# Performance work log

Hardware: AMD Instinct MI355X
Metric: run time of the kernel (lower is better)

The kernel has to match this reference:

```python
import jax, jax.numpy as jnp
import numpy as np

B, T, C = 2, 2048, 1024
NH = 16
HD = C // NH

def setup_inputs() -> dict:
    key = jax.random.key(0)
    ks = jax.random.split(key, 4)
    x = jax.random.normal(ks[0], (B, T, C), dtype=jnp.float32)
    w_attn = jax.random.normal(ks[1], (C, 3 * C), dtype=jnp.float32) * (1.0 / np.sqrt(C))
    b_attn = jnp.zeros((3 * C,), dtype=jnp.float32)
    w_proj = jax.random.normal(ks[2], (C, C), dtype=jnp.float32) * (1.0 / np.sqrt(C))
    b_proj = jnp.zeros((C,), dtype=jnp.float32)
    return {"x": x, "w_attn": w_attn, "b_attn": b_attn, "w_proj": w_proj, "b_proj": b_proj}

def reference(x, w_attn, b_attn, w_proj, b_proj):
    Bq, Tq, Cq = x.shape
    qkv = x @ w_attn + b_attn                      # [B,T,3C]
    q, k, v = jnp.split(qkv, 3, axis=2)
    # [B,T,C] -> [B,NH,T,HD]
    def heads(t):
        return t.reshape(Bq, Tq, NH, HD).transpose(0, 2, 1, 3)
    q, k, v = heads(q), heads(k), heads(v)
    att = jnp.einsum('bhqd,bhkd->bhqk', q, k) * (1.0 / np.sqrt(HD))
    causal = jnp.tril(jnp.ones((Tq, Tq), dtype=bool))
    att = jnp.where(causal[None, None], att, -jnp.inf)
    att = jax.nn.softmax(att, axis=-1)
    y = jnp.einsum('bhqk,bhkd->bhqd', att, v)      # [B,NH,T,HD]
    y = y.transpose(0, 2, 1, 3).reshape(Bq, Tq, Cq)
    return y @ w_proj + b_proj
```

## Files before the change

### kernel.cpp

```cpp
#include <hip/hip_runtime.h>

typedef unsigned short u16;
typedef short bf16x8 __attribute__((ext_vector_type(8)));
typedef float f32x4 __attribute__((ext_vector_type(4)));

#define BATCH 2
#define SEQ   2048
#define CH    1024
#define NHEAD 16
#define HDIM  64
#define ROWS  (BATCH*SEQ)

#define WAITV(N) asm volatile("s_waitcnt vmcnt(" #N ")" ::: "memory")

__device__ __forceinline__ u16 f2b(float f) {
  unsigned u = __builtin_bit_cast(unsigned, f);
  u += 0x7FFFu + ((u >> 16) & 1u);
  return (u16)(u >> 16);
}
__device__ __forceinline__ float b2f(u16 h) {
  unsigned u = ((unsigned)h) << 16;
  return __builtin_bit_cast(float, u);
}
__device__ __forceinline__ float exp2_fast(float x) {
  float r; asm("v_exp_f32 %0, %1" : "=v"(r) : "v"(x)); return r;
}
__device__ __forceinline__ unsigned cvt_pk_bf16(float a, float b) {
  unsigned r; asm("v_cvt_pk_bf16_f32 %0, %1, %2" : "=v"(r) : "v"(a), "v"(b)); return r;
}

__device__ __forceinline__ void gload_lds16(const void* g, void* l) {
  __builtin_amdgcn_global_load_lds(
      (const __attribute__((address_space(1))) unsigned int*)g,
      (__attribute__((address_space(3))) unsigned int*)l, 16, 0, 0);
}

__global__ void csa_prep(const float* __restrict__ x,
                         const float* __restrict__ wa, const float* __restrict__ wp,
                         u16* __restrict__ xb, u16* __restrict__ wat,
                         u16* __restrict__ wpt) {
  __shared__ float tile[32][33];
  const int b = blockIdx.x, t = threadIdx.x;
  if (b < 2048) {
    int i = b * 256 + t;
    const float4* f4 = (const float4*)x;
    float4 v0 = f4[2*i], v1 = f4[2*i+1];
    ushort4 o0, o1;
    o0.x = f2b(v0.x); o0.y = f2b(v0.y); o0.z = f2b(v0.z); o0.w = f2b(v0.w);
    o1.x = f2b(v1.x); o1.y = f2b(v1.y); o1.z = f2b(v1.z); o1.w = f2b(v1.w);
    ((ushort4*)xb)[2*i]   = o0;
    ((ushort4*)xb)[2*i+1] = o1;
    return;
  }
  int bb = b - 2048;
  int bx = bb & 127, by = bb >> 7;
  const float* in; u16* out; int C;
  if (bx < 96) { in = wa; out = wat; C = 3*CH; }
  else         { in = wp; out = wpt; C = CH; bx -= 96; }
  const int R = CH;
  const int bxc = bx * 32, byc = by * 32;
  const int tx = t & 31, ty = t >> 5;
  #pragma unroll
  for (int j = 0; j < 4; ++j) {
    int r = byc + ty + j*8, c = bxc + tx;
    tile[ty + j*8][tx] = in[(size_t)r*C + c];
  }
  __syncthreads();
  #pragma unroll
  for (int j = 0; j < 4; ++j) {
    int oc = bxc + ty + j*8;
    int orr = byc + tx;
    out[(size_t)oc*R + orr] = f2b(tile[tx][ty + j*8]);
  }
}

__global__ __launch_bounds__(512) void csa_gemm_qkv(
    const u16* __restrict__ A, const u16* __restrict__ Bt,
    const float* __restrict__ bias,
    u16* __restrict__ qbo, u16* __restrict__ kb, u16* __restrict__ vtb)
{
  __shared__ __align__(16) u16 As[3][256*64];
  __shared__ __align__(16) u16 Bs[2][192*64];
  const int t = threadIdx.x, lane = t & 63, w = t >> 6;
  const int wm = w >> 2, wn = w & 3, g = lane >> 4, qi = lane & 15;
  const int xq = (qi & 7) * 8;

  const int wgid = blockIdx.y * 16 + blockIdx.x;
  const int c8 = wgid & 7, inner = wgid >> 3;
  const int bm = (c8 >> 1) * 4 + (inner >> 3);
  const int bn = (c8 & 1) * 8 + (inner & 7);

  f32x4 acc[8][3] = {};

  const u16* Ab = A  + (size_t)(bm*256)*CH;
  const u16* Bb = Bt + (size_t)(bn*192)*CH;
  const int srow = t >> 3;
  const int scolsw = ((t & 7) * 8) ^ ((srow & 7) * 8);

#define QKV_STAGE_A(kt_, buf_) do { const size_t k_ = (size_t)(kt_)*64;            \
    gload_lds16(Ab + (size_t)(  0 + srow)*CH + k_ + scolsw, &As[buf_][      w*512]); \
    gload_lds16(Ab + (size_t)( 64 + srow)*CH + k_ + scolsw, &As[buf_][ 4096+w*512]); \
    gload_lds16(Ab + (size_t)(128 + srow)*CH + k_ + scolsw, &As[buf_][ 8192+w*512]); \
    gload_lds16(Ab + (size_t)(192 + srow)*CH + k_ + scolsw, &As[buf_][12288+w*512]); \
  } while (0)
#define QKV_STAGE_B(kt_, buf_) do { const size_t k_ = (size_t)(kt_)*64;            \
    gload_lds16(Bb + (size_t)(  0 + srow)*CH + k_ + scolsw, &Bs[buf_][      w*512]); \
    gload_lds16(Bb + (size_t)( 64 + srow)*CH + k_ + scolsw, &Bs[buf_][ 4096+w*512]); \
    gload_lds16(Bb + (size_t)(128 + srow)*CH + k_ + scolsw, &Bs[buf_][ 8192+w*512]); \
  } while (0)

  QKV_STAGE_A(0, 0); QKV_STAGE_B(0, 0); QKV_STAGE_A(1, 1);

  int a3 = 0;
  for (int kt = 0; kt < 16; ++kt) {
    if (kt < 15) QKV_STAGE_B(kt + 1, (kt + 1) & 1);
    if (kt < 14) { int ab = a3 + 2; if (ab >= 3) ab -= 3; QKV_STAGE_A(kt + 2, ab); }
    if (kt < 14)       WAITV(11);
    else if (kt == 14) WAITV(7);
    else               WAITV(0);
    __builtin_amdgcn_s_barrier();
    __builtin_amdgcn_sched_barrier(0);
    const u16* Ac = &As[a3][0];
    const u16* Bc = &Bs[kt & 1][0];
    #pragma unroll
    for (int kk = 0; kk < 2; ++kk) {
      bf16x8 af[8], bfr[3];
      #pragma unroll
      for (int m = 0; m < 8; ++m)
        af[m] = *(const bf16x8*)&Ac[(wm*128 + m*16 + qi)*64 + ((kk*32 + g*8) ^ xq)];
      #pragma unroll
      for (int n = 0; n < 3; ++n)
        bfr[n] = *(const bf16x8*)&Bc[(wn*48 + n*16 + qi)*64 + ((kk*32 + g*8) ^ xq)];
      #pragma unroll
      for (int m = 0; m < 8; ++m)
        #pragma unroll
        for (int n = 0; n < 3; ++n)
          acc[m][n] = __builtin_amdgcn_mfma_f32_16x16x32_bf16(af[m], bfr[n], acc[m][n], 0, 0, 0);
    }
    __builtin_amdgcn_s_barrier();
    a3 = (a3 == 2) ? 0 : a3 + 1;
  }
#undef QKV_STAGE_A
#undef QKV_STAGE_B

  #pragma unroll
  for (int m = 0; m < 8; ++m) {
    const int row0 = bm*256 + wm*128 + m*16 + g*4;
    const int bb = row0 >> 11;
    const int t0 = row0 & 2047;
    #pragma unroll
    for (int n = 0; n < 3; ++n) {
      const int col = bn*192 + wn*48 + n*16 + qi;
      const float bv = bias[col];
      const int which = col >> 10;
      const int cc = col & 1023;
      const int h = cc >> 6, d = cc & 63;
      const int bh = bb*16 + h;
      if (which == 2) {
        ushort4 pw;
        pw.x = f2b(acc[m][n][0] + bv);
        pw.y = f2b(acc[m][n][1] + bv);
        pw.z = f2b(acc[m][n][2] + bv);
        pw.w = f2b(acc[m][n][3] + bv);
        *(ushort4*)&vtb[((size_t)bh*HDIM + d)*SEQ + t0] = pw;
      } else {
        u16* dst = (which == 0) ? qbo : kb;
        #pragma unroll
        for (int r = 0; r < 4; ++r)
          dst[((size_t)bh*SEQ + t0 + r)*HDIM + d] = f2b(acc[m][n][r] + bv);
      }
    }
  }
}

__global__ __launch_bounds__(256) void csa_gemm_proj(
    const u16* __restrict__ A, const u16* __restrict__ Bt,
    const float* __restrict__ bias, float* __restrict__ out)
{
  __shared__ __align__(16) u16 As[3][128*64];
  __shared__ __align__(16) u16 Bs[2][128*64];
  const int t = threadIdx.x, lane = t & 63, w = t >> 6;
  const int wm = w >> 1, wn = w & 1, g = lane >> 4, qi = lane & 15;
  const int xq = (qi & 7) * 8;
  const int bm = blockIdx.y, bn = blockIdx.x;

  f32x4 acc[4][4] = {};

  const u16* Ab = A  + (size_t)(bm*128)*CH;
  const u16* Bb = Bt + (size_t)(bn*128)*CH;
  const int srow = t >> 3;
  const int scolsw = ((t & 7) * 8) ^ ((srow & 7) * 8);

#define PRJ_STAGE(P_, base_, kt_, buf_) do { const size_t k_ = (size_t)(kt_)*64;      \
    gload_lds16(P_ + (size_t)( 0 + srow)*CH + k_ + scolsw, &base_[buf_][     w*512]); \
    gload_lds16(P_ + (size_t)(32 + srow)*CH + k_ + scolsw, &base_[buf_][2048+w*512]); \
    gload_lds16(P_ + (size_t)(64 + srow)*CH + k_ + scolsw, &base_[buf_][4096+w*512]); \
    gload_lds16(P_ + (size_t)(96 + srow)*CH + k_ + scolsw, &base_[buf_][6144+w*512]); \
  } while (0)

  PRJ_STAGE(Ab, As, 0, 0); PRJ_STAGE(Bb, Bs, 0, 0); PRJ_STAGE(Ab, As, 1, 1);

  int a3 = 0;
  for (int kt = 0; kt < 16; ++kt) {
    if (kt < 15) PRJ_STAGE(Bb, Bs, kt + 1, (kt + 1) & 1);
    if (kt < 14) { int ab = a3 + 2; if (ab >= 3) ab -= 3; PRJ_STAGE(Ab, As, kt + 2, ab); }
    if (kt < 14)       WAITV(12);
    else if (kt == 14) WAITV(8);
    else               WAITV(0);
    __builtin_amdgcn_s_barrier();
    __builtin_amdgcn_sched_barrier(0);
    const u16* Ac = &As[a3][0];
    const u16* Bc = &Bs[kt & 1][0];
    #pragma unroll
    for (int kk = 0; kk < 2; ++kk) {
      bf16x8 af[4], bfr[4];
      #pragma unroll
      for (int m = 0; m < 4; ++m)
        af[m] = *(const bf16x8*)&Ac[(wm*64 + m*16 + qi)*64 + ((kk*32 + g*8) ^ xq)];
      #pragma unroll
      for (int n = 0; n < 4; ++n)
        bfr[n] = *(const bf16x8*)&Bc[(wn*64 + n*16 + qi)*64 + ((kk*32 + g*8) ^ xq)];
      #pragma unroll
      for (int m = 0; m < 4; ++m)
        #pragma unroll
        for (int n = 0; n < 4; ++n)
          acc[m][n] = __builtin_amdgcn_mfma_f32_16x16x32_bf16(af[m], bfr[n], acc[m][n], 0, 0, 0);
    }
    __builtin_amdgcn_s_barrier();
    a3 = (a3 == 2) ? 0 : a3 + 1;
  }
#undef PRJ_STAGE

  #pragma unroll
  for (int m = 0; m < 4; ++m) {
    const int row0 = bm*128 + wm*64 + m*16 + g*4;
    #pragma unroll
    for (int n = 0; n < 4; ++n) {
      const int col = bn*128 + wn*64 + n*16 + qi;
      const float bv = bias[col];
      #pragma unroll
      for (int r = 0; r < 4; ++r)
        out[(size_t)(row0 + r)*CH + col] = acc[m][n][r] + bv;
    }
  }
}

__global__ __launch_bounds__(512) void csa_attn(
    const u16* __restrict__ qb, const u16* __restrict__ kb,
    const u16* __restrict__ vtb, u16* __restrict__ yout)
{
  const int bh = blockIdx.x, pair = blockIdx.y;
  const int bidx = bh >> 4, h = bh & 15;
  const int t = threadIdx.x, lane = t & 63, w = t >> 6;
  const int g = lane >> 4, qi = lane & 15;
  __shared__ __align__(16) u16 Ks[2][128*64];
  __shared__ __align__(16) u16 Vs[2][64*128];
  __shared__ __align__(16) u16 Ps[8][2][16*64];

  const size_t kvbase = (size_t)bh * SEQ * HDIM;
  const u16* kb_bh  = kb  + kvbase;
  const u16* vtb_bh = vtb + kvbase;

  const int krow_  = t >> 3;
  const int kcolsw = ((t & 7) * 8) ^ ((krow_ & 7) * 8);
  const int vd_    = t >> 4;
  const int vcolsw = ((t & 15) * 8) ^ ((vd_ & 15) * 8);

  int offKb[2][4], offVb[2][4], offPw[4], offPr[2];
  #pragma unroll
  for (int c = 0; c < 2; ++c) {
    offPr[c] = qi*64 + ((c*32 + g*8) ^ ((qi & 7) * 8));
    #pragma unroll
    for (int s4 = 0; s4 < 4; ++s4)
      offKb[c][s4] = (s4*16 + qi)*64 + ((c*32 + g*8) ^ ((qi & 7) * 8));
    #pragma unroll
    for (int nf = 0; nf < 4; ++nf)
      offVb[c][nf] = (nf*16 + qi)*128 + ((c*32 + g*8) ^ (qi * 8));
  }
  #pragma unroll
  for (int s4 = 0; s4 < 4; ++s4)
    offPw[s4] = qi*64 + ((s4*16 + g*4) ^ ((qi & 7) * 8));

  const float QSCALE = 0.18033688011112042f;
  const int lqa = w*16 + qi;

  for (int half = 0; half < 2; ++half) {
    const int qt = half ? (15 - pair) : pair;
    const int qrow = qt*128 + w*16;
    const int ntile = qt + 1;

    bf16x8 qf[2];
    #pragma unroll
    for (int c = 0; c < 2; ++c) {
      qf[c] = *(const bf16x8*)&qb[(kvbase + (size_t)(qrow + qi)*HDIM) + c*32 + g*8];
      #pragma unroll
      for (int e = 0; e < 8; ++e)
        qf[c][e] = (short)f2b(b2f((u16)qf[c][e]) * QSCALE);
    }

    f32x4 yacc[4] = {};
    float mrun = -1e30f, srun = 0.f;

    __syncthreads();
    {
      const u16* kp = kb_bh;
      gload_lds16(kp + (size_t)krow_*64 + kcolsw,        &Ks[0][       w*512]);
      gload_lds16(kp + (size_t)(64 + krow_)*64 + kcolsw, &Ks[0][4096 + w*512]);
      const u16* vp = vtb_bh;
      gload_lds16(vp + (size_t)vd_*SEQ + vcolsw,         &Vs[0][       w*512]);
      gload_lds16(vp + (size_t)(32 + vd_)*SEQ + vcolsw,  &Vs[0][4096 + w*512]);
    }
    __syncthreads();

    int buf = 0;
    for (int kt = 0; kt < ntile; ++kt) {
      if (kt + 1 < ntile) {
        const u16* kp = kb_bh + (size_t)((kt + 1) * 128) * 64;
        gload_lds16(kp + (size_t)krow_*64 + kcolsw,        &Ks[buf^1][       w*512]);
        gload_lds16(kp + (size_t)(64 + krow_)*64 + kcolsw, &Ks[buf^1][4096 + w*512]);
        const u16* vp = vtb_bh + (kt + 1) * 128;
        gload_lds16(vp + (size_t)vd_*SEQ + vcolsw,         &Vs[buf^1][       w*512]);
        gload_lds16(vp + (size_t)(32 + vd_)*SEQ + vcolsw,  &Vs[buf^1][4096 + w*512]);
      }

      f32x4 sa[4] = {}, sb[4] = {};
      #pragma unroll
      for (int c = 0; c < 2; ++c)
        #pragma unroll
        for (int s4 = 0; s4 < 4; ++s4) {
          bf16x8 ka = *(const bf16x8*)&Ks[buf][offKb[c][s4]];
          sa[s4] = __builtin_amdgcn_mfma_f32_16x16x32_bf16(ka, qf[c], sa[s4], 0, 0, 0);
        }
      #pragma unroll
      for (int c = 0; c < 2; ++c)
        #pragma unroll
        for (int s4 = 0; s4 < 4; ++s4) {
          bf16x8 kbv = *(const bf16x8*)&Ks[buf][4096 + offKb[c][s4]];
          sb[s4] = __builtin_amdgcn_mfma_f32_16x16x32_bf16(kbv, qf[c], sb[s4], 0, 0, 0);
        }

      if (kt == ntile - 1) {
        #pragma unroll
        for (int s4 = 0; s4 < 4; ++s4)
          #pragma unroll
          for (int r = 0; r < 4; ++r) {
            const int lk = s4*16 + g*4 + r;
            if (lk > lqa)      sa[s4][r] = -3.0e38f;
            if (lk > lqa - 64) sb[s4][r] = -3.0e38f;
          }
      }

      float tmax = sa[0][0];
      #pragma unroll
      for (int s4 = 0; s4 < 4; ++s4)
        #pragma unroll
        for (int r = 0; r < 4; ++r) {
          tmax = fmaxf(tmax, sa[s4][r]);
          tmax = fmaxf(tmax, sb[s4][r]);
        }
      if (!__all(tmax - mrun <= 11.5f)) {
        float tmf = fmaxf(tmax, __shfl_xor(tmax, 16));
        tmf = fmaxf(tmf, __shfl_xor(tmf, 32));
        float mnew = fmaxf(mrun, tmf);
        float fac = exp2_fast(mrun - mnew);
        #pragma unroll
        for (int r = 0; r < 4; ++r) {
          float fr = __shfl(fac, g*4 + r);
          #pragma unroll
          for (int nf = 0; nf < 4; ++nf) yacc[nf][r] *= fr;
        }
        srun *= fac;
        mrun = mnew;
      }
      float tsum = 0.f;
      #pragma unroll
      for (int s4 = 0; s4 < 4; ++s4)
        #pragma unroll
        for (int r = 0; r < 4; ++r) {
          float pa = exp2_fast(sa[s4][r] - mrun);
          float pb = exp2_fast(sb[s4][r] - mrun);
          sa[s4][r] = pa; sb[s4][r] = pb;
          tsum += pa + pb;
        }
      srun += tsum;

      #pragma unroll
      for (int s4 = 0; s4 < 4; ++s4) {
        uint2 pwa, pwb;
        pwa.x = cvt_pk_bf16(sa[s4][0], sa[s4][1]);
        pwa.y = cvt_pk_bf16(sa[s4][2], sa[s4][3]);
        pwb.x = cvt_pk_bf16(sb[s4][0], sb[s4][1]);
        pwb.y = cvt_pk_bf16(sb[s4][2], sb[s4][3]);
        *(uint2*)&Ps[w][0][offPw[s4]] = pwa;
        *(uint2*)&Ps[w][1][offPw[s4]] = pwb;
      }

      #pragma unroll
      for (int c = 0; c < 2; ++c) {
        bf16x8 pa0 = *(const bf16x8*)&Ps[w][0][offPr[c]];
        bf16x8 pb0 = *(const bf16x8*)&Ps[w][1][offPr[c]];
        #pragma unroll
        for (int nf = 0; nf < 4; ++nf) {
          bf16x8 va = *(const bf16x8*)&Vs[buf][offVb[c][nf]];
          yacc[nf] = __builtin_amdgcn_mfma_f32_16x16x32_bf16(pa0, va, yacc[nf], 0, 0, 0);
          bf16x8 vb = *(const bf16x8*)&Vs[buf][offVb[c][nf] ^ 64];
          yacc[nf] = __builtin_amdgcn_mfma_f32_16x16x32_bf16(pb0, vb, yacc[nf], 0, 0, 0);
        }
      }

      __syncthreads();
      buf ^= 1;
    }

    float srf = srun + __shfl_xor(srun, 16);
    srf += __shfl_xor(srf, 32);
    #pragma unroll
    for (int r = 0; r < 4; ++r) {
      float sv = __shfl(srf, g*4 + r);
      float inv = 1.f / sv;
      int qg = qrow + g*4 + r;
      #pragma unroll
      for (int nf = 0; nf < 4; ++nf) {
        int d = nf*16 + qi;
        yout[((size_t)bidx*SEQ + qg)*CH + h*HDIM + d] = f2b(yacc[nf][r] * inv);
      }
    }
  }
}

extern "C" void kernel_launch(void* const* d_in, const int* in_sizes, int n_in,
                              void* d_out, int out_size, void* d_ws, size_t ws_size,
                              hipStream_t stream) {
  (void)in_sizes; (void)n_in; (void)out_size; (void)ws_size;
  const float* x      = (const float*)d_in[0];
  const float* w_attn = (const float*)d_in[1];
  const float* b_attn = (const float*)d_in[2];
  const float* w_proj = (const float*)d_in[3];
  const float* b_proj = (const float*)d_in[4];

  char* ws = (char*)d_ws;
  const size_t MB = 1024*1024;
  u16* xb  = (u16*)(ws);
  u16* wat = (u16*)(ws +  8*MB);
  u16* wpt = (u16*)(ws + 14*MB);
  u16* qb  = (u16*)(ws + 16*MB);
  u16* kb  = (u16*)(ws + 24*MB);
  u16* vtb = (u16*)(ws + 32*MB);

  csa_prep<<<6144, 256, 0, stream>>>(x, w_attn, w_proj, xb, wat, wpt);
  csa_gemm_qkv<<<dim3(16, 16), 512, 0, stream>>>(xb, wat, b_attn, qb, kb, vtb);
  csa_attn<<<dim3(32, 8), 512, 0, stream>>>(qb, kb, vtb, xb);
  csa_gemm_proj<<<dim3(8, 32), 256, 0, stream>>>(xb, wpt, b_proj, (float*)d_out);
}
```

Baseline: 99.24 us.

## Triple-buffer attention K/V tiles with vmcnt waits and MFMA priority boosts

Result: no change. 100.5 us (+1.2%).

```diff
diff --git a/kernel.cpp b/kernel.cpp
--- a/kernel.cpp
+++ b/kernel.cpp
@@ -253,8 +253,8 @@
   const int bidx = bh >> 4, h = bh & 15;
   const int t = threadIdx.x, lane = t & 63, w = t >> 6;
   const int g = lane >> 4, qi = lane & 15;
-  __shared__ __align__(16) u16 Ks[2][128*64];
-  __shared__ __align__(16) u16 Vs[2][64*128];
+  __shared__ __align__(16) u16 Ks[3][128*64];
+  __shared__ __align__(16) u16 Vs[3][64*128];
   __shared__ __align__(16) u16 Ps[8][2][16*64];
 
   const size_t kvbase = (size_t)bh * SEQ * HDIM;
@@ -266,6 +266,15 @@
   const int vd_    = t >> 4;
   const int vcolsw = ((t & 15) * 8) ^ ((vd_ & 15) * 8);
 
+#define ATTN_STAGE(kt_, buf_) do {                                                  \
+    const u16* kp_ = kb_bh + (size_t)((kt_) * 128) * 64;                            \
+    gload_lds16(kp_ + (size_t)krow_*64 + kcolsw,        &Ks[buf_][       w*512]);   \
+    gload_lds16(kp_ + (size_t)(64 + krow_)*64 + kcolsw, &Ks[buf_][4096 + w*512]);   \
+    const u16* vp_ = vtb_bh + (kt_) * 128;                                          \
+    gload_lds16(vp_ + (size_t)vd_*SEQ + vcolsw,         &Vs[buf_][       w*512]);   \
+    gload_lds16(vp_ + (size_t)(32 + vd_)*SEQ + vcolsw,  &Vs[buf_][4096 + w*512]);   \
+  } while (0)
+
   int offKb[2][4], offVb[2][4], offPw[4], offPr[2];
   #pragma unroll
   for (int c = 0; c < 2; ++c) {
@@ -301,43 +310,38 @@
     f32x4 yacc[4] = {};
     float mrun = -1e30f, srun = 0.f;
 
-    __syncthreads();
-    {
-      const u16* kp = kb_bh;
-      gload_lds16(kp + (size_t)krow_*64 + kcolsw,        &Ks[0][       w*512]);
-      gload_lds16(kp + (size_t)(64 + krow_)*64 + kcolsw, &Ks[0][4096 + w*512]);
-      const u16* vp = vtb_bh;
-      gload_lds16(vp + (size_t)vd_*SEQ + vcolsw,         &Vs[0][       w*512]);
-      gload_lds16(vp + (size_t)(32 + vd_)*SEQ + vcolsw,  &Vs[0][4096 + w*512]);
-    }
-    __syncthreads();
-
-    int buf = 0;
+    ATTN_STAGE(0, 0);
+    if (ntile > 1) ATTN_STAGE(1, 1);
+
+    int cur = 0;
     for (int kt = 0; kt < ntile; ++kt) {
-      if (kt + 1 < ntile) {
-        const u16* kp = kb_bh + (size_t)((kt + 1) * 128) * 64;
-        gload_lds16(kp + (size_t)krow_*64 + kcolsw,        &Ks[buf^1][       w*512]);
-        gload_lds16(kp + (size_t)(64 + krow_)*64 + kcolsw, &Ks[buf^1][4096 + w*512]);
-        const u16* vp = vtb_bh + (kt + 1) * 128;
-        gload_lds16(vp + (size_t)vd_*SEQ + vcolsw,         &Vs[buf^1][       w*512]);
-        gload_lds16(vp + (size_t)(32 + vd_)*SEQ + vcolsw,  &Vs[buf^1][4096 + w*512]);
-      }
+      {
+        int b2 = cur + 2; if (b2 >= 3) b2 -= 3;
+        if (kt + 2 < ntile) ATTN_STAGE(kt + 2, b2);
+      }
+      if (kt + 2 < ntile)      WAITV(8);
+      else if (kt + 1 < ntile) WAITV(4);
+      else                     WAITV(0);
+      __builtin_amdgcn_s_barrier();
+      __builtin_amdgcn_sched_barrier(0);
 
       f32x4 sa[4] = {}, sb[4] = {};
+      __builtin_amdgcn_s_setprio(1);
       #pragma unroll
       for (int c = 0; c < 2; ++c)
         #pragma unroll
         for (int s4 = 0; s4 < 4; ++s4) {
-          bf16x8 ka = *(const bf16x8*)&Ks[buf][offKb[c][s4]];
+          bf16x8 ka = *(const bf16x8*)&Ks[cur][offKb[c][s4]];
           sa[s4] = __builtin_amdgcn_mfma_f32_16x16x32_bf16(ka, qf[c], sa[s4], 0, 0, 0);
         }
       #pragma unroll
       for (int c = 0; c < 2; ++c)
         #pragma unroll
         for (int s4 = 0; s4 < 4; ++s4) {
-          bf16x8 kbv = *(const bf16x8*)&Ks[buf][4096 + offKb[c][s4]];
+          bf16x8 kbv = *(const bf16x8*)&Ks[cur][4096 + offKb[c][s4]];
           sb[s4] = __builtin_amdgcn_mfma_f32_16x16x32_bf16(kbv, qf[c], sb[s4], 0, 0, 0);
         }
+      __builtin_amdgcn_s_setprio(0);
 
       if (kt == ntile - 1) {
         #pragma unroll
@@ -395,22 +399,25 @@
         *(uint2*)&Ps[w][1][offPw[s4]] = pwb;
       }
 
+      __builtin_amdgcn_s_setprio(1);
       #pragma unroll
       for (int c = 0; c < 2; ++c) {
         bf16x8 pa0 = *(const bf16x8*)&Ps[w][0][offPr[c]];
         bf16x8 pb0 = *(const bf16x8*)&Ps[w][1][offPr[c]];
         #pragma unroll
         for (int nf = 0; nf < 4; ++nf) {
-          bf16x8 va = *(const bf16x8*)&Vs[buf][offVb[c][nf]];
+          bf16x8 va = *(const bf16x8*)&Vs[cur][offVb[c][nf]];
           yacc[nf] = __builtin_amdgcn_mfma_f32_16x16x32_bf16(pa0, va, yacc[nf], 0, 0, 0);
-          bf16x8 vb = *(const bf16x8*)&Vs[buf][offVb[c][nf] ^ 64];
+          bf16x8 vb = *(const bf16x8*)&Vs[cur][offVb[c][nf] ^ 64];
           yacc[nf] = __builtin_amdgcn_mfma_f32_16x16x32_bf16(pb0, vb, yacc[nf], 0, 0, 0);
         }
       }
-
-      __syncthreads();
-      buf ^= 1;
-    }
+      __builtin_amdgcn_s_setprio(0);
+
+      __builtin_amdgcn_s_barrier();
+      cur = (cur == 2) ? 0 : cur + 1;
+    }
+#undef ATTN_STAGE
 
     float srf = srun + __shfl_xor(srun, 16);
     srf += __shfl_xor(srf, 32);
```

## Rework attention kernel with 32x32 MFMA, register P, and split-KV wave pairs

Applied to the files above, without the earlier changes.

New measurement: 104.9 us. +5.7%, slower.

```diff
diff --git a/kernel.cpp b/kernel.cpp
--- a/kernel.cpp
+++ b/kernel.cpp
@@ -3,6 +3,7 @@
 typedef unsigned short u16;
 typedef short bf16x8 __attribute__((ext_vector_type(8)));
 typedef float f32x4 __attribute__((ext_vector_type(4)));
+typedef float f32x16 __attribute__((ext_vector_type(16)));
 
 #define BATCH 2
 #define SEQ   2048
@@ -252,180 +253,180 @@
   const int bh = blockIdx.x, pair = blockIdx.y;
   const int bidx = bh >> 4, h = bh & 15;
   const int t = threadIdx.x, lane = t & 63, w = t >> 6;
-  const int g = lane >> 4, qi = lane & 15;
+  const int j = w >> 1, sub = w & 1;
+  const int l31 = lane & 31, hi = lane >> 5;
+
   __shared__ __align__(16) u16 Ks[2][128*64];
   __shared__ __align__(16) u16 Vs[2][64*128];
-  __shared__ __align__(16) u16 Ps[8][2][16*64];
+  __shared__ float mtab[8][32], stab[8][32], ftab[8][32];
 
   const size_t kvbase = (size_t)bh * SEQ * HDIM;
   const u16* kb_bh  = kb  + kvbase;
   const u16* vtb_bh = vtb + kvbase;
 
-  const int krow_  = t >> 3;
-  const int kcolsw = ((t & 7) * 8) ^ ((krow_ & 7) * 8);
-  const int vd_    = t >> 4;
-  const int vcolsw = ((t & 15) * 8) ^ ((vd_ & 15) * 8);
-
-  int offKb[2][4], offVb[2][4], offPw[4], offPr[2];
-  #pragma unroll
-  for (int c = 0; c < 2; ++c) {
-    offPr[c] = qi*64 + ((c*32 + g*8) ^ ((qi & 7) * 8));
-    #pragma unroll
-    for (int s4 = 0; s4 < 4; ++s4)
-      offKb[c][s4] = (s4*16 + qi)*64 + ((c*32 + g*8) ^ ((qi & 7) * 8));
-    #pragma unroll
-    for (int nf = 0; nf < 4; ++nf)
-      offVb[c][nf] = (nf*16 + qi)*128 + ((c*32 + g*8) ^ (qi * 8));
-  }
-  #pragma unroll
-  for (int s4 = 0; s4 < 4; ++s4)
-    offPw[s4] = qi*64 + ((s4*16 + g*4) ^ ((qi & 7) * 8));
+  const int krow = t >> 3;
+  const int kcol = 8 * ((t & 7) ^ (krow & 7));
+  const int vrow = t >> 4;
+  const int vcol = 8 * ((t & 15) ^ (vrow & 15));
+
+#define ATTN_STAGE(kt_, b_) do {                                             \
+    const u16* kp_ = kb_bh + (size_t)((kt_)*128 + krow)*64 + kcol;           \
+    gload_lds16(kp_,           &Ks[b_][       w*512]);                       \
+    gload_lds16(kp_ + 64*64,   &Ks[b_][4096 + w*512]);                       \
+    const u16* vp_ = vtb_bh + (size_t)vrow*SEQ + (kt_)*128 + vcol;           \
+    gload_lds16(vp_,           &Vs[b_][       w*512]);                       \
+    gload_lds16(vp_ + 32*SEQ,  &Vs[b_][4096 + w*512]);                       \
+  } while (0)
+
+  int offK[2][4];
+  #pragma unroll
+  for (int kb2 = 0; kb2 < 2; ++kb2)
+    #pragma unroll
+    for (int ds = 0; ds < 4; ++ds)
+      offK[kb2][ds] = (sub*64 + kb2*32 + l31)*64 + ((ds*16 + hi*8) ^ ((l31 & 7)*8));
+  int offV[2][4];
+  #pragma unroll
+  for (int db = 0; db < 2; ++db)
+    #pragma unroll
+    for (int ks = 0; ks < 4; ++ks)
+      offV[db][ks] = (db*32 + l31)*128 + (((sub*8 + 2*ks + hi) ^ (l31 & 15))*8);
+
+#define PACK(ps_, b_, out_) do {                                             \
+    unsigned A0_ = cvt_pk_bf16(ps_[(b_)+0], ps_[(b_)+1]);                    \
+    unsigned A1_ = cvt_pk_bf16(ps_[(b_)+2], ps_[(b_)+3]);                    \
+    unsigned B0_ = cvt_pk_bf16(ps_[(b_)+4], ps_[(b_)+5]);                    \
+    unsigned B1_ = cvt_pk_bf16(ps_[(b_)+6], ps_[(b_)+7]);                    \
+    asm volatile("v_permlane32_swap_b32 %0, %1" : "+v"(A0_), "+v"(B0_));     \
+    asm volatile("v_permlane32_swap_b32 %0, %1" : "+v"(A1_), "+v"(B1_));     \
+    union { unsigned u[4]; bf16x8 v; } pu_;                                  \
+    pu_.u[0] = A0_; pu_.u[1] = A1_; pu_.u[2] = B0_; pu_.u[3] = B1_;          \
+    out_ = pu_.v;                                                            \
+  } while (0)
 
   const float QSCALE = 0.18033688011112042f;
-  const int lqa = w*16 + qi;
+  const int qloc = j*32 + l31;
 
   for (int half = 0; half < 2; ++half) {
     const int qt = half ? (15 - pair) : pair;
-    const int qrow = qt*128 + w*16;
     const int ntile = qt + 1;
-
-    bf16x8 qf[2];
-    #pragma unroll
-    for (int c = 0; c < 2; ++c) {
-      qf[c] = *(const bf16x8*)&qb[(kvbase + (size_t)(qrow + qi)*HDIM) + c*32 + g*8];
+    const int qrow = qt*128 + j*32;
+
+    bf16x8 qf[4];
+    #pragma unroll
+    for (int ds = 0; ds < 4; ++ds) {
+      qf[ds] = *(const bf16x8*)&qb[kvbase + (size_t)(qrow + l31)*HDIM + ds*16 + hi*8];
       #pragma unroll
       for (int e = 0; e < 8; ++e)
-        qf[c][e] = (short)f2b(b2f((u16)qf[c][e]) * QSCALE);
-    }
-
-    f32x4 yacc[4] = {};
+        qf[ds][e] = (short)f2b(b2f((u16)qf[ds][e]) * QSCALE);
+    }
+
+    f32x16 yacc0 = {}, yacc1 = {};
     float mrun = -1e30f, srun = 0.f;
 
-    __syncthreads();
-    {
-      const u16* kp = kb_bh;
-      gload_lds16(kp + (size_t)krow_*64 + kcolsw,        &Ks[0][       w*512]);
-      gload_lds16(kp + (size_t)(64 + krow_)*64 + kcolsw, &Ks[0][4096 + w*512]);
-      const u16* vp = vtb_bh;
-      gload_lds16(vp + (size_t)vd_*SEQ + vcolsw,         &Vs[0][       w*512]);
-      gload_lds16(vp + (size_t)(32 + vd_)*SEQ + vcolsw,  &Vs[0][4096 + w*512]);
-    }
+    ATTN_STAGE(0, 0);
     __syncthreads();
 
     int buf = 0;
     for (int kt = 0; kt < ntile; ++kt) {
-      if (kt + 1 < ntile) {
-        const u16* kp = kb_bh + (size_t)((kt + 1) * 128) * 64;
-        gload_lds16(kp + (size_t)krow_*64 + kcolsw,        &Ks[buf^1][       w*512]);
-        gload_lds16(kp + (size_t)(64 + krow_)*64 + kcolsw, &Ks[buf^1][4096 + w*512]);
-        const u16* vp = vtb_bh + (kt + 1) * 128;
-        gload_lds16(vp + (size_t)vd_*SEQ + vcolsw,         &Vs[buf^1][       w*512]);
-        gload_lds16(vp + (size_t)(32 + vd_)*SEQ + vcolsw,  &Vs[buf^1][4096 + w*512]);
-      }
-
-      f32x4 sa[4] = {}, sb[4] = {};
-      #pragma unroll
-      for (int c = 0; c < 2; ++c)
-        #pragma unroll
-        for (int s4 = 0; s4 < 4; ++s4) {
-          bf16x8 ka = *(const bf16x8*)&Ks[buf][offKb[c][s4]];
-          sa[s4] = __builtin_amdgcn_mfma_f32_16x16x32_bf16(ka, qf[c], sa[s4], 0, 0, 0);
-        }
-      #pragma unroll
-      for (int c = 0; c < 2; ++c)
-        #pragma unroll
-        for (int s4 = 0; s4 < 4; ++s4) {
-          bf16x8 kbv = *(const bf16x8*)&Ks[buf][4096 + offKb[c][s4]];
-          sb[s4] = __builtin_amdgcn_mfma_f32_16x16x32_bf16(kbv, qf[c], sb[s4], 0, 0, 0);
-        }
+      if (kt + 1 < ntile) ATTN_STAGE(kt + 1, buf ^ 1);
+
+      f32x16 s0 = {}, s1 = {};
+      #pragma unroll
+      for (int ds = 0; ds < 4; ++ds) {
+        bf16x8 k0 = *(const bf16x8*)&Ks[buf][offK[0][ds]];
+        s0 = __builtin_amdgcn_mfma_f32_32x32x16_bf16(k0, qf[ds], s0, 0, 0, 0);
+        bf16x8 k1 = *(const bf16x8*)&Ks[buf][offK[1][ds]];
+        s1 = __builtin_amdgcn_mfma_f32_32x32x16_bf16(k1, qf[ds], s1, 0, 0, 0);
+      }
 
       if (kt == ntile - 1) {
         #pragma unroll
-        for (int s4 = 0; s4 < 4; ++s4)
-          #pragma unroll
-          for (int r = 0; r < 4; ++r) {
-            const int lk = s4*16 + g*4 + r;
-            if (lk > lqa)      sa[s4][r] = -3.0e38f;
-            if (lk > lqa - 64) sb[s4][r] = -3.0e38f;
-          }
-      }
-
-      float tmax = sa[0][0];
-      #pragma unroll
-      for (int s4 = 0; s4 < 4; ++s4)
-        #pragma unroll
-        for (int r = 0; r < 4; ++r) {
-          tmax = fmaxf(tmax, sa[s4][r]);
-          tmax = fmaxf(tmax, sb[s4][r]);
+        for (int reg = 0; reg < 16; ++reg) {
+          const int cr = (reg & 3) + 8*(reg >> 2) + 4*hi;
+          if (sub*64 + cr > qloc)      s0[reg] = -3.0e38f;
+          if (sub*64 + 32 + cr > qloc) s1[reg] = -3.0e38f;
         }
+      }
+
+      float tmax = fmaxf(s0[0], s1[0]);
+      #pragma unroll
+      for (int reg = 1; reg < 16; ++reg)
+        tmax = fmaxf(tmax, fmaxf(s0[reg], s1[reg]));
       if (!__all(tmax - mrun <= 11.5f)) {
-        float tmf = fmaxf(tmax, __shfl_xor(tmax, 16));
-        tmf = fmaxf(tmf, __shfl_xor(tmf, 32));
+        float tmf = fmaxf(tmax, __shfl_xor(tmax, 32));
         float mnew = fmaxf(mrun, tmf);
         float fac = exp2_fast(mrun - mnew);
+        if (lane < 32) ftab[w][l31] = fac;
         #pragma unroll
-        for (int r = 0; r < 4; ++r) {
-          float fr = __shfl(fac, g*4 + r);
-          #pragma unroll
-          for (int nf = 0; nf < 4; ++nf) yacc[nf][r] *= fr;
+        for (int reg = 0; reg < 16; ++reg) {
+          float fr = ftab[w][(reg & 3) + 8*(reg >> 2) + 4*hi];
+          yacc0[reg] *= fr; yacc1[reg] *= fr;
         }
-        srun *= fac;
-        mrun = mnew;
+        srun *= fac; mrun = mnew;
       }
       float tsum = 0.f;
       #pragma unroll
-      for (int s4 = 0; s4 < 4; ++s4)
-        #pragma unroll
-        for (int r = 0; r < 4; ++r) {
-          float pa = exp2_fast(sa[s4][r] - mrun);
-          float pb = exp2_fast(sb[s4][r] - mrun);
-          sa[s4][r] = pa; sb[s4][r] = pb;
-          tsum += pa + pb;
-        }
+      for (int reg = 0; reg < 16; ++reg) {
+        float p0 = exp2_fast(s0[reg] - mrun);
+        float p1 = exp2_fast(s1[reg] - mrun);
+        s0[reg] = p0; s1[reg] = p1;
+        tsum += p0 + p1;
+      }
       srun += tsum;
 
-      #pragma unroll
-      for (int s4 = 0; s4 < 4; ++s4) {
-        uint2 pwa, pwb;
-        pwa.x = cvt_pk_bf16(sa[s4][0], sa[s4][1]);
-        pwa.y = cvt_pk_bf16(sa[s4][2], sa[s4][3]);
-        pwb.x = cvt_pk_bf16(sb[s4][0], sb[s4][1]);
-        pwb.y = cvt_pk_bf16(sb[s4][2], sb[s4][3]);
-        *(uint2*)&Ps[w][0][offPw[s4]] = pwa;
-        *(uint2*)&Ps[w][1][offPw[s4]] = pwb;
-      }
-
-      #pragma unroll
-      for (int c = 0; c < 2; ++c) {
-        bf16x8 pa0 = *(const bf16x8*)&Ps[w][0][offPr[c]];
-        bf16x8 pb0 = *(const bf16x8*)&Ps[w][1][offPr[c]];
-        #pragma unroll
-        for (int nf = 0; nf < 4; ++nf) {
-          bf16x8 va = *(const bf16x8*)&Vs[buf][offVb[c][nf]];
-          yacc[nf] = __builtin_amdgcn_mfma_f32_16x16x32_bf16(pa0, va, yacc[nf], 0, 0, 0);
-          bf16x8 vb = *(const bf16x8*)&Vs[buf][offVb[c][nf] ^ 64];
-          yacc[nf] = __builtin_amdgcn_mfma_f32_16x16x32_bf16(pb0, vb, yacc[nf], 0, 0, 0);
-        }
-      }
+      bf16x8 pa0, pa1, pa2, pa3;
+      PACK(s0, 0, pa0); PACK(s0, 8, pa1); PACK(s1, 0, pa2); PACK(s1, 8, pa3);
+
+      yacc0 = __builtin_amdgcn_mfma_f32_32x32x16_bf16(pa0, *(const bf16x8*)&Vs[buf][offV[0][0]], yacc0, 0, 0, 0);
+      yacc0 = __builtin_amdgcn_mfma_f32_32x32x16_bf16(pa1, *(const bf16x8*)&Vs[buf][offV[0][1]], yacc0, 0, 0, 0);
+      yacc0 = __builtin_amdgcn_mfma_f32_32x32x16_bf16(pa2, *(const bf16x8*)&Vs[buf][offV[0][2]], yacc0, 0, 0, 0);
+      yacc0 = __builtin_amdgcn_mfma_f32_32x32x16_bf16(pa3, *(const bf16x8*)&Vs[buf][offV[0][3]], yacc0, 0, 0, 0);
+      yacc1 = __builtin_amdgcn_mfma_f32_32x32x16_bf16(pa0, *(const bf16x8*)&Vs[buf][offV[1][0]], yacc1, 0, 0, 0);
+      yacc1 = __builtin_amdgcn_mfma_f32_32x32x16_bf16(pa1, *(const bf16x8*)&Vs[buf][offV[1][1]], yacc1, 0, 0, 0);
+      yacc1 = __builtin_amdgcn_mfma_f32_32x32x16_bf16(pa2, *(const bf16x8*)&Vs[buf][offV[1][2]], yacc1, 0, 0, 0);
+      yacc1 = __builtin_amdgcn_mfma_f32_32x32x16_bf16(pa3, *(const bf16x8*)&Vs[buf][offV[1][3]], yacc1, 0, 0, 0);
 
       __syncthreads();
       buf ^= 1;
     }
 
-    float srf = srun + __shfl_xor(srun, 16);
-    srf += __shfl_xor(srf, 32);
-    #pragma unroll
-    for (int r = 0; r < 4; ++r) {
-      float sv = __shfl(srf, g*4 + r);
-      float inv = 1.f / sv;
-      int qg = qrow + g*4 + r;
-      #pragma unroll
-      for (int nf = 0; nf < 4; ++nf) {
-        int d = nf*16 + qi;
-        yout[((size_t)bidx*SEQ + qg)*CH + h*HDIM + d] = f2b(yacc[nf][r] * inv);
-      }
-    }
-  }
+    float sfull = srun + __shfl_xor(srun, 32);
+    if (lane < 32) { mtab[w][l31] = mrun; stab[w][l31] = sfull; }
+    __syncthreads();
+
+    float* Ocomb = (float*)&Ks[0][0];
+    const int wA = w & ~1, wB = w | 1;
+    if (sub == 1) {
+      #pragma unroll
+      for (int reg = 0; reg < 16; ++reg) {
+        const int cr = (reg & 3) + 8*(reg >> 2) + 4*hi;
+        float mA = mtab[wA][cr], mB = mtab[wB][cr];
+        float fB = exp2_fast(mB - fmaxf(mA, mB));
+        Ocomb[(j*32 + cr)*64 +      l31] = yacc0[reg] * fB;
+        Ocomb[(j*32 + cr)*64 + 32 + l31] = yacc1[reg] * fB;
+      }
+    }
+    __syncthreads();
+    if (sub == 0) {
+      #pragma unroll
+      for (int reg = 0; reg < 16; ++reg) {
+        const int cr = (reg & 3) + 8*(reg >> 2) + 4*hi;
+        float mA = mtab[wA][cr], mB = mtab[wB][cr];
+        float sA = stab[wA][cr], sB = stab[wB][cr];
+        float ms = fmaxf(mA, mB);
+        float fA = exp2_fast(mA - ms), fB = exp2_fast(mB - ms);
+        float inv = 1.f / (sA * fA + sB * fB);
+        const size_t orow = ((size_t)bidx*SEQ + qt*128 + j*32 + cr)*CH + h*HDIM;
+        float v0 = (yacc0[reg] * fA + Ocomb[(j*32 + cr)*64 +      l31]) * inv;
+        float v1 = (yacc1[reg] * fA + Ocomb[(j*32 + cr)*64 + 32 + l31]) * inv;
+        yout[orow +      l31] = f2b(v0);
+        yout[orow + 32 + l31] = f2b(v1);
+      }
+    }
+    __syncthreads();
+  }
+#undef ATTN_STAGE
+#undef PACK
 }
 
 extern "C" void kernel_launch(void* const* d_in, const int* in_sizes, int n_in,
```

## Widen attention KV tile to 256 keys with single reusable P buffer

Applied to the files above, without the earlier changes.

Result: slower. 104.3 us (+5.1%).

```diff
diff --git a/kernel.cpp b/kernel.cpp
--- a/kernel.cpp
+++ b/kernel.cpp
@@ -253,33 +253,53 @@
   const int bidx = bh >> 4, h = bh & 15;
   const int t = threadIdx.x, lane = t & 63, w = t >> 6;
   const int g = lane >> 4, qi = lane & 15;
-  __shared__ __align__(16) u16 Ks[2][128*64];
-  __shared__ __align__(16) u16 Vs[2][64*128];
-  __shared__ __align__(16) u16 Ps[8][2][16*64];
+  __shared__ __align__(16) u16 Ks[2][256*64];
+  __shared__ __align__(16) u16 Vs[2][64*256];
+  __shared__ __align__(16) u16 Ps[8][16*64];
 
   const size_t kvbase = (size_t)bh * SEQ * HDIM;
   const u16* kb_bh  = kb  + kvbase;
   const u16* vtb_bh = vtb + kvbase;
 
-  const int krow_  = t >> 3;
-  const int kcolsw = ((t & 7) * 8) ^ ((krow_ & 7) * 8);
-  const int vd_    = t >> 4;
-  const int vcolsw = ((t & 15) * 8) ^ ((vd_ & 15) * 8);
-
-  int offKb[2][4], offVb[2][4], offPw[4], offPr[2];
+  const int krow4  = t >> 3;
+  const int kcolsw = ((t & 7) * 8) ^ ((krow4 & 7) * 8);
+  const int vrow16 = t >> 5;
+  const int vcolsw0 = 8 * ((t & 31) ^ vrow16);
+  const int vcolsw1 = 8 * ((t & 31) ^ (16 + vrow16));
+
+#define ATTN_STAGE(kbase_, b_) do {                                               \
+    const u16* kp_ = kb_bh + (size_t)((kbase_) + krow4)*64;                       \
+    gload_lds16(kp_ +            kcolsw, &Ks[b_][       w*512]);                  \
+    gload_lds16(kp_ +  64*64  + kcolsw, &Ks[b_][ 4096 + w*512]);                  \
+    gload_lds16(kp_ + 128*64  + kcolsw, &Ks[b_][ 8192 + w*512]);                  \
+    gload_lds16(kp_ + 192*64  + kcolsw, &Ks[b_][12288 + w*512]);                  \
+    const u16* vp_ = vtb_bh + (size_t)vrow16*SEQ + (kbase_);                      \
+    gload_lds16(vp_ +           vcolsw0, &Vs[b_][       w*512]);                  \
+    gload_lds16(vp_ + 16*SEQ + vcolsw1, &Vs[b_][ 4096 + w*512]);                  \
+    gload_lds16(vp_ + 32*SEQ + vcolsw0, &Vs[b_][ 8192 + w*512]);                  \
+    gload_lds16(vp_ + 48*SEQ + vcolsw1, &Vs[b_][12288 + w*512]);                  \
+  } while (0)
+
+  int offKb[2][4], offPw[4], offPr[2];
   #pragma unroll
   for (int c = 0; c < 2; ++c) {
     offPr[c] = qi*64 + ((c*32 + g*8) ^ ((qi & 7) * 8));
     #pragma unroll
     for (int s4 = 0; s4 < 4; ++s4)
       offKb[c][s4] = (s4*16 + qi)*64 + ((c*32 + g*8) ^ ((qi & 7) * 8));
-    #pragma unroll
-    for (int nf = 0; nf < 4; ++nf)
-      offVb[c][nf] = (nf*16 + qi)*128 + ((c*32 + g*8) ^ (qi * 8));
   }
   #pragma unroll
   for (int s4 = 0; s4 < 4; ++s4)
     offPw[s4] = qi*64 + ((s4*16 + g*4) ^ ((qi & 7) * 8));
+  int offVb[4][2][4];
+  #pragma unroll
+  for (int s = 0; s < 4; ++s)
+    #pragma unroll
+    for (int c = 0; c < 2; ++c)
+      #pragma unroll
+      for (int nf = 0; nf < 4; ++nf)
+        offVb[s][c][nf] = (nf*16 + qi)*256 +
+                          (((s*8 + c*4 + g) ^ (((nf & 1)*16) + qi)) * 8);
 
   const float QSCALE = 0.18033688011112042f;
   const int lqa = w*16 + qi;
@@ -287,7 +307,7 @@
   for (int half = 0; half < 2; ++half) {
     const int qt = half ? (15 - pair) : pair;
     const int qrow = qt*128 + w*16;
-    const int ntile = qt + 1;
+    const int ntile = (qt + 2) >> 1;
 
     bf16x8 qf[2];
     #pragma unroll
@@ -300,64 +320,56 @@
 
     f32x4 yacc[4] = {};
     float mrun = -1e30f, srun = 0.f;
+    const int dq = 128*qt - 256*(ntile - 1) + lqa;
 
     __syncthreads();
-    {
-      const u16* kp = kb_bh;
-      gload_lds16(kp + (size_t)krow_*64 + kcolsw,        &Ks[0][       w*512]);
-      gload_lds16(kp + (size_t)(64 + krow_)*64 + kcolsw, &Ks[0][4096 + w*512]);
-      const u16* vp = vtb_bh;
-      gload_lds16(vp + (size_t)vd_*SEQ + vcolsw,         &Vs[0][       w*512]);
-      gload_lds16(vp + (size_t)(32 + vd_)*SEQ + vcolsw,  &Vs[0][4096 + w*512]);
-    }
+    ATTN_STAGE(0, 0);
     __syncthreads();
 
     int buf = 0;
     for (int kt = 0; kt < ntile; ++kt) {
-      if (kt + 1 < ntile) {
-        const u16* kp = kb_bh + (size_t)((kt + 1) * 128) * 64;
-        gload_lds16(kp + (size_t)krow_*64 + kcolsw,        &Ks[buf^1][       w*512]);
-        gload_lds16(kp + (size_t)(64 + krow_)*64 + kcolsw, &Ks[buf^1][4096 + w*512]);
-        const u16* vp = vtb_bh + (kt + 1) * 128;
-        gload_lds16(vp + (size_t)vd_*SEQ + vcolsw,         &Vs[buf^1][       w*512]);
-        gload_lds16(vp + (size_t)(32 + vd_)*SEQ + vcolsw,  &Vs[buf^1][4096 + w*512]);
+      if (kt + 1 < ntile) ATTN_STAGE((kt + 1) * 256, buf ^ 1);
+
+      f32x4 S[4][4];
+      #pragma unroll
+      for (int s = 0; s < 4; ++s)
+        #pragma unroll
+        for (int s4 = 0; s4 < 4; ++s4)
+          S[s][s4] = (f32x4){0.f, 0.f, 0.f, 0.f};
+      #pragma unroll
+      for (int s = 0; s < 4; ++s)
+        #pragma unroll
+        for (int c = 0; c < 2; ++c)
+          #pragma unroll
+          for (int s4 = 0; s4 < 4; ++s4) {
+            bf16x8 kf = *(const bf16x8*)&Ks[buf][s*4096 + offKb[c][s4]];
+            S[s][s4] = __builtin_amdgcn_mfma_f32_16x16x32_bf16(kf, qf[c], S[s][s4], 0, 0, 0);
+          }
+
+      if (kt == ntile - 1) {
+        #pragma unroll
+        for (int s = 0; s < 4; ++s)
+          #pragma unroll
+          for (int s4 = 0; s4 < 4; ++s4)
+            #pragma unroll
+            for (int r = 0; r < 4; ++r) {
+              const int lkrel = s*64 + s4*16 + g*4 + r;
+              if (lkrel > dq) S[s][s4][r] = -3.0e38f;
+            }
       }
 
-      f32x4 sa[4] = {}, sb[4] = {};
-      #pragma unroll
-      for (int c = 0; c < 2; ++c)
+      float a0 = S[0][0][0], a1 = S[0][0][1], a2 = S[0][0][2], a3 = S[0][0][3];
+      #pragma unroll
+      for (int s = 0; s < 4; ++s)
         #pragma unroll
         for (int s4 = 0; s4 < 4; ++s4) {
-          bf16x8 ka = *(const bf16x8*)&Ks[buf][offKb[c][s4]];
-          sa[s4] = __builtin_amdgcn_mfma_f32_16x16x32_bf16(ka, qf[c], sa[s4], 0, 0, 0);
+          if (s == 0 && s4 == 0) continue;
+          a0 = fmaxf(a0, S[s][s4][0]);
+          a1 = fmaxf(a1, S[s][s4][1]);
+          a2 = fmaxf(a2, S[s][s4][2]);
+          a3 = fmaxf(a3, S[s][s4][3]);
         }
-      #pragma unroll
-      for (int c = 0; c < 2; ++c)
-        #pragma unroll
-        for (int s4 = 0; s4 < 4; ++s4) {
-          bf16x8 kbv = *(const bf16x8*)&Ks[buf][4096 + offKb[c][s4]];
-          sb[s4] = __builtin_amdgcn_mfma_f32_16x16x32_bf16(kbv, qf[c], sb[s4], 0, 0, 0);
-        }
-
-      if (kt == ntile - 1) {
-        #pragma unroll
-        for (int s4 = 0; s4 < 4; ++s4)
-          #pragma unroll
-          for (int r = 0; r < 4; ++r) {
-            const int lk = s4*16 + g*4 + r;
-            if (lk > lqa)      sa[s4][r] = -3.0e38f;
-            if (lk > lqa - 64) sb[s4][r] = -3.0e38f;
-          }
-      }
-
-      float tmax = sa[0][0];
-      #pragma unroll
-      for (int s4 = 0; s4 < 4; ++s4)
-        #pragma unroll
-        for (int r = 0; r < 4; ++r) {
-          tmax = fmaxf(tmax, sa[s4][r]);
-          tmax = fmaxf(tmax, sb[s4][r]);
-        }
+      float tmax = fmaxf(fmaxf(a0, a1), fmaxf(a2, a3));
       if (!__all(tmax - mrun <= 11.5f)) {
         float tmf = fmaxf(tmax, __shfl_xor(tmax, 16));
         tmf = fmaxf(tmf, __shfl_xor(tmf, 32));
@@ -374,37 +386,34 @@
       }
       float tsum = 0.f;
       #pragma unroll
-      for (int s4 = 0; s4 < 4; ++s4)
-        #pragma unroll
-        for (int r = 0; r < 4; ++r) {
-          float pa = exp2_fast(sa[s4][r] - mrun);
-          float pb = exp2_fast(sb[s4][r] - mrun);
-          sa[s4][r] = pa; sb[s4][r] = pb;
-          tsum += pa + pb;
+      for (int s = 0; s < 4; ++s)
+        #pragma unroll
+        for (int s4 = 0; s4 < 4; ++s4)
+          #pragma unroll
+          for (int r = 0; r < 4; ++r) {
+            float p = exp2_fast(S[s][s4][r] - mrun);
+            S[s][s4][r] = p;
+            tsum += p;
+          }
+      srun += tsum;
+
+      #pragma unroll
+      for (int s = 0; s < 4; ++s) {
+        #pragma unroll
+        for (int s4 = 0; s4 < 4; ++s4) {
+          uint2 pw;
+          pw.x = cvt_pk_bf16(S[s][s4][0], S[s][s4][1]);
+          pw.y = cvt_pk_bf16(S[s][s4][2], S[s][s4][3]);
+          *(uint2*)&Ps[w][offPw[s4]] = pw;
         }
-      srun += tsum;
-
-      #pragma unroll
-      for (int s4 = 0; s4 < 4; ++s4) {
-        uint2 pwa, pwb;
-        pwa.x = cvt_pk_bf16(sa[s4][0], sa[s4][1]);
-        pwa.y = cvt_pk_bf16(sa[s4][2], sa[s4][3]);
-        pwb.x = cvt_pk_bf16(sb[s4][0], sb[s4][1]);
-        pwb.y = cvt_pk_bf16(sb[s4][2], sb[s4][3]);
-        *(uint2*)&Ps[w][0][offPw[s4]] = pwa;
-        *(uint2*)&Ps[w][1][offPw[s4]] = pwb;
-      }
-
-      #pragma unroll
-      for (int c = 0; c < 2; ++c) {
-        bf16x8 pa0 = *(const bf16x8*)&Ps[w][0][offPr[c]];
-        bf16x8 pb0 = *(const bf16x8*)&Ps[w][1][offPr[c]];
-        #pragma unroll
-        for (int nf = 0; nf < 4; ++nf) {
-          bf16x8 va = *(const bf16x8*)&Vs[buf][offVb[c][nf]];
-          yacc[nf] = __builtin_amdgcn_mfma_f32_16x16x32_bf16(pa0, va, yacc[nf], 0, 0, 0);
-          bf16x8 vb = *(const bf16x8*)&Vs[buf][offVb[c][nf] ^ 64];
-          yacc[nf] = __builtin_amdgcn_mfma_f32_16x16x32_bf16(pb0, vb, yacc[nf], 0, 0, 0);
+        #pragma unroll
+        for (int c = 0; c < 2; ++c) {
+          bf16x8 pa = *(const bf16x8*)&Ps[w][offPr[c]];
+          #pragma unroll
+          for (int nf = 0; nf < 4; ++nf) {
+            bf16x8 vf = *(const bf16x8*)&Vs[buf][offVb[s][c][nf]];
+            yacc[nf] = __builtin_amdgcn_mfma_f32_16x16x32_bf16(pa, vf, yacc[nf], 0, 0, 0);
+          }
         }
       }
 
@@ -426,6 +435,7 @@
       }
     }
   }
+#undef ATTN_STAGE
 }
 
 extern "C" void kernel_launch(void* const* d_in, const int* in_sizes, int n_in,
```
